# Performance work log

Hardware: AMD Instinct MI355X
Metric: run time of the kernel (lower is better)

## Reference

```python
import jax, jax.numpy as jnp
import numpy as np

N, E, B, T = 50000, 800000, 256, 50
IN_DIM, H, C1, C2, Q_DIM, LH = 128, 4, 32, 128, 32, 128
EPS = 1e-5


def setup_inputs() -> dict:
    key = jax.random.key(0)
    ks = jax.random.split(key, 24)
    g = 0.05
    inp = {
        'x': jax.random.normal(ks[0], (N, IN_DIM), jnp.float32),
        'edge_index': jax.random.randint(ks[1], (2, E), 0, N, jnp.int32),
        'batch': jnp.sort(jax.random.randint(ks[2], (N,), 0, B, jnp.int32)),
        'quant': jax.random.normal(ks[3], (B, T, Q_DIM), jnp.float32),
        # GATConv(128 -> 32, heads=4, concat)
        'gat_W': jax.random.normal(ks[4], (IN_DIM, H * C1), jnp.float32) * g,
        'gat_att_src': jax.random.normal(ks[5], (H, C1), jnp.float32) * g,
        'gat_att_dst': jax.random.normal(ks[6], (H, C1), jnp.float32) * g,
        'gat_b': jnp.zeros((H * C1,), jnp.float32),
        # BN1 over 128 channels (eval mode)
        'bn1_gamma': jnp.ones((H * C1,), jnp.float32),
        'bn1_beta': jnp.zeros((H * C1,), jnp.float32),
        'bn1_mean': jax.random.normal(ks[7], (H * C1,), jnp.float32) * 0.01,
        'bn1_var': jnp.ones((H * C1,), jnp.float32),
        # GCNConv(128 -> 128)
        'gcn_W': jax.random.normal(ks[8], (H * C1, C2), jnp.float32) * g,
        'gcn_b': jnp.zeros((C2,), jnp.float32),
        'bn2_gamma': jnp.ones((C2,), jnp.float32),
        'bn2_beta': jnp.zeros((C2,), jnp.float32),
        'bn2_mean': jax.random.normal(ks[9], (C2,), jnp.float32) * 0.01,
        'bn2_var': jnp.ones((C2,), jnp.float32),
        # GlobalAttention gate: Linear(C2 -> 1)
        'gate_W': jax.random.normal(ks[10], (1, C2), jnp.float32) * g,
        'gate_b': jnp.zeros((1,), jnp.float32),
        # LSTM(Q_DIM -> LH), torch gate order i,f,g,o
        'lstm_Wih': jax.random.normal(ks[11], (4 * LH, Q_DIM), jnp.float32) * g,
        'lstm_Whh': jax.random.normal(ks[12], (4 * LH, LH), jnp.float32) * g,
        'lstm_bih': jnp.zeros((4 * LH,), jnp.float32),
        'lstm_bhh': jnp.zeros((4 * LH,), jnp.float32),
        # final Linear(C2+LH -> 1)
        'fc_W': jax.random.normal(ks[13], (1, C2 + LH), jnp.float32) * g,
        'fc_b': jnp.zeros((1,), jnp.float32),
    }
    return inp


def _segment_softmax(e, seg, num_segments):
    m = jax.ops.segment_max(e, seg, num_segments=num_segments)
    ex = jnp.exp(e - m[seg])
    s = jax.ops.segment_sum(ex, seg, num_segments=num_segments)
    return ex / (s[seg] + 1e-16)


def _bn_eval(x, gamma, beta, mean, var):
    return gamma * (x - mean) * jax.lax.rsqrt(var + EPS) + beta


def _forward(x, edge_index, batch, quant,
             gat_W, gat_att_src, gat_att_dst, gat_b,
             bn1_gamma, bn1_beta, bn1_mean, bn1_var,
             gcn_W, gcn_b, bn2_gamma, bn2_beta, bn2_mean, bn2_var,
             gate_W, gate_b,
             lstm_Wih, lstm_Whh, lstm_bih, lstm_bhh,
             fc_W, fc_b):
    n = x.shape[0]
    loops = jnp.arange(n, dtype=edge_index.dtype)
    ei = jnp.concatenate([edge_index, jnp.stack([loops, loops])], axis=1)  # add self loops
    src, dst = ei[0], ei[1]

    # ---- GATConv ----
    xw = (x @ gat_W).reshape(n, H, C1)                      # [N,H,C1]
    a_src = jnp.sum(xw * gat_att_src, axis=-1)              # [N,H]
    a_dst = jnp.sum(xw * gat_att_dst, axis=-1)
    e = jax.nn.leaky_relu(a_src[src] + a_dst[dst], 0.2)     # [E+N,H]
    alpha = _segment_softmax(e, dst, n)                     # softmax over in-edges per dst
    msg = xw[src] * alpha[:, :, None]                       # [E+N,H,C1]
    h = jax.ops.segment_sum(msg, dst, num_segments=n).reshape(n, H * C1) + gat_b

    h = jax.nn.elu(h)
    h = _bn_eval(h, bn1_gamma, bn1_beta, bn1_mean, bn1_var)

    # ---- GCNConv (sym-normalized with self loops) ----
    deg = jax.ops.segment_sum(jnp.ones_like(dst, jnp.float32), dst, num_segments=n)
    dinv = jnp.where(deg > 0, jax.lax.rsqrt(deg), 0.0)
    norm = dinv[src] * dinv[dst]                            # [E+N]
    hw = h @ gcn_W                                          # [N,C2]
    h2 = jax.ops.segment_sum(hw[src] * norm[:, None], dst, num_segments=n) + gcn_b

    h2 = jax.nn.elu(h2)
    h2 = _bn_eval(h2, bn2_gamma, bn2_beta, bn2_mean, bn2_var)

    # ---- GlobalAttention pooling over graphs ----
    gate = (h2 @ gate_W.T + gate_b)[:, 0]                   # [N]
    score = _segment_softmax(gate, batch, B)
    graph_rep = jax.ops.segment_sum(score[:, None] * h2, batch, num_segments=B)  # [B,C2]

    # ---- LSTM over quant series ----
    def step(carry, xt):
        hh, cc = carry
        gates = xt @ lstm_Wih.T + hh @ lstm_Whh.T + lstm_bih + lstm_bhh
        i, f, gg, o = jnp.split(gates, 4, axis=-1)
        cc = jax.nn.sigmoid(f) * cc + jax.nn.sigmoid(i) * jnp.tanh(gg)
        hh = jax.nn.sigmoid(o) * jnp.tanh(cc)
        return (hh, cc), None

    h0 = jnp.zeros((B, LH), quant.dtype)
    (hT, _), _ = jax.lax.scan(step, (h0, h0), jnp.swapaxes(quant, 0, 1))

    combined = jnp.concatenate([graph_rep, hT], axis=1)     # [B, C2+LH]
    out = (combined @ fc_W.T + fc_b)[:, 0]                  # [B]
    return out


def reference(x, edge_index, batch, quant,
              gat_W, gat_att_src, gat_att_dst, gat_b,
              bn1_gamma, bn1_beta, bn1_mean, bn1_var,
              gcn_W, gcn_b, bn2_gamma, bn2_beta, bn2_mean, bn2_var,
              gate_W, gate_b,
              lstm_Wih, lstm_Whh, lstm_bih, lstm_bhh,
              fc_W, fc_b):
    return _forward(x, edge_index, batch, quant,
                    gat_W, gat_att_src, gat_att_dst, gat_b,
                    bn1_gamma, bn1_beta, bn1_mean, bn1_var,
                    gcn_W, gcn_b, bn2_gamma, bn2_beta, bn2_mean, bn2_var,
                    gate_W, gate_b,
                    lstm_Wih, lstm_Whh, lstm_bih, lstm_bhh,
                    fc_W, fc_b)
```

## Files before the change

### kernel.cpp

```cpp
#include <hip/hip_runtime.h>
#include <cfloat>
#include <cstddef>

constexpr int KIN   = 128;
constexpr int KQD   = 32;
constexpr int KT    = 50;
constexpr int KLH   = 128;
constexpr float BN_EPS = 1e-5f;

typedef __attribute__((ext_vector_type(8))) short bf16x8;
typedef __attribute__((ext_vector_type(4))) float f32x4;
union U8 { bf16x8 v; unsigned u[4]; };

__device__ __forceinline__ float elu_f(float x)  { return x > 0.f ? x : expm1f(x); }
__device__ __forceinline__ float leaky_f(float x){ return x > 0.f ? x : 0.2f * x; }
__device__ __forceinline__ float fsigm(float x)  { return 1.f / (1.f + __expf(-x)); }
__device__ __forceinline__ float ftanh(float x)  { return 1.f - 2.f / (__expf(2.f * x) + 1.f); }

__device__ __forceinline__ unsigned bfpack(float lo, float hi) {
    unsigned ul = __float_as_uint(lo), uh = __float_as_uint(hi);
    ul += 0x7FFFu + ((ul >> 16) & 1u);
    uh += 0x7FFFu + ((uh >> 16) & 1u);
    return (ul >> 16) | (uh & 0xFFFF0000u);
}
__device__ __forceinline__ unsigned short bf1(float v) {
    unsigned u = __float_as_uint(v);
    u += 0x7FFFu + ((u >> 16) & 1u);
    return (unsigned short)(u >> 16);
}
__device__ __forceinline__ float bflo(unsigned u) { return __uint_as_float(u << 16); }
__device__ __forceinline__ float bfhi(unsigned u) { return __uint_as_float(u & 0xFFFF0000u); }

__device__ __forceinline__ bf16x8 pack8(float4 p, float4 q) {
    U8 t;
    t.u[0] = bfpack(p.x, p.y); t.u[1] = bfpack(p.z, p.w);
    t.u[2] = bfpack(q.x, q.y); t.u[3] = bfpack(q.z, q.w);
    return t.v;
}

__global__ void k_deg(const int* __restrict__ ei, int E, int* __restrict__ deg) {
    int e = blockIdx.x * blockDim.x + threadIdx.x;
    if (e < E) atomicAdd(&deg[ei[E + e]], 1);
}

__global__ __launch_bounds__(1024)
void k_scan(const int* __restrict__ deg, int n, int* __restrict__ offsets,
            int* __restrict__ cursor, float* __restrict__ dinv) {
    __shared__ int wsum[16];
    __shared__ int carry_sh;
    int tid = threadIdx.x, lane = tid & 63, w = tid >> 6;
    if (tid == 0) { carry_sh = 0; offsets[0] = 0; }
    __syncthreads();
    for (int base = 0; base < n; base += 4096) {
        int i0 = base + tid * 4;
        int v[4];
        #pragma unroll
        for (int j = 0; j < 4; j++) v[j] = (i0 + j < n) ? deg[i0 + j] : 0;
        int tsum = v[0] + v[1] + v[2] + v[3];
        int sc = tsum;
        #pragma unroll
        for (int d = 1; d < 64; d <<= 1) {
            int o = __shfl_up(sc, d);
            if (lane >= d) sc += o;
        }
        __syncthreads();
        if (lane == 63) wsum[w] = sc;
        __syncthreads();
        if (w == 0) {
            int xx = (lane < 16) ? wsum[lane] : 0;
            #pragma unroll
            for (int d = 1; d < 16; d <<= 1) {
                int o = __shfl_up(xx, d);
                if (lane >= d) xx += o;
            }
            if (lane < 16) wsum[lane] = xx;
        }
        __syncthreads();
        int carry = carry_sh;
        int woff  = (w > 0) ? wsum[w - 1] : 0;
        int run   = carry + woff + sc - tsum;
        #pragma unroll
        for (int j = 0; j < 4; j++) {
            int i = i0 + j;
            if (i < n) {
                cursor[i]      = run;
                offsets[i + 1] = run + v[j];
                dinv[i]        = rsqrtf((float)(v[j] + 1));
                run += v[j];
            }
        }
        __syncthreads();
        if (tid == 0) carry_sh = carry + wsum[15];
    }
}

__global__ void k_fill(const int* __restrict__ ei, int E, int* __restrict__ cursor,
                       int* __restrict__ csr_src) {
    int e = blockIdx.x * blockDim.x + threadIdx.x;
    if (e < E) {
        int s = ei[e], d = ei[E + e];
        int pos = atomicAdd(&cursor[d], 1);
        csr_src[pos] = s;
    }
}

template <bool ATT>
__global__ __launch_bounds__(256, 4)
void k_gemm_mfma(const float* __restrict__ X, const float* __restrict__ W,
                 unsigned* __restrict__ Yb, int nrows,
                 const float* __restrict__ attS, const float* __restrict__ attD,
                 float* __restrict__ a_src, float* __restrict__ a_dst) {
    __shared__ float tile[16][132];
    __shared__ float as_sh[128], ad_sh[128];
    int tid  = threadIdx.x;
    int lane = tid & 63;
    int wv   = tid >> 6;
    if (ATT && tid < 128) { as_sh[tid] = attS[tid]; ad_sh[tid] = attD[tid]; }
    int l16 = lane & 15;
    int kq  = (lane >> 4) * 8;
    bf16x8 bfr[2][4];
    #pragma unroll
    for (int nt = 0; nt < 2; nt++) {
        int n = wv * 32 + nt * 16 + l16;
        #pragma unroll
        for (int kk = 0; kk < 4; kk++) {
            int k0 = kk * 32 + kq;
            float f[8];
            #pragma unroll
            for (int j = 0; j < 8; j++) f[j] = W[(size_t)(k0 + j) * 128 + n];
            U8 t;
            t.u[0] = bfpack(f[0], f[1]); t.u[1] = bfpack(f[2], f[3]);
            t.u[2] = bfpack(f[4], f[5]); t.u[3] = bfpack(f[6], f[7]);
            bfr[nt][kk] = t.v;
        }
    }
    int nch = (nrows + 15) / 16;
    for (int ch = blockIdx.x; ch < nch; ch += gridDim.x) {
        int r0 = ch * 16;
        int r  = r0 + l16;
        bool rok = r < nrows;
        const float* xr = X + (size_t)r * 128 + kq;
        float4 z4 = make_float4(0.f, 0.f, 0.f, 0.f);
        bf16x8 afr[4];
        #pragma unroll
        for (int kk = 0; kk < 4; kk++) {
            float4 p = rok ? *reinterpret_cast<const float4*>(xr + kk * 32)     : z4;
            float4 q = rok ? *reinterpret_cast<const float4*>(xr + kk * 32 + 4) : z4;
            afr[kk] = pack8(p, q);
        }
        f32x4 acc0 = {0.f, 0.f, 0.f, 0.f};
        f32x4 acc1 = {0.f, 0.f, 0.f, 0.f};
        #pragma unroll
        for (int kk = 0; kk < 4; kk++) {
            acc0 = __builtin_amdgcn_mfma_f32_16x16x32_bf16(afr[kk], bfr[0][kk], acc0, 0, 0, 0);
            acc1 = __builtin_amdgcn_mfma_f32_16x16x32_bf16(afr[kk], bfr[1][kk], acc1, 0, 0, 0);
        }
        __syncthreads();
        int rowb = (lane >> 4) * 4;
        int cb   = wv * 32 + l16;
        #pragma unroll
        for (int reg = 0; reg < 4; reg++) {
            tile[rowb + reg][cb]      = acc0[reg];
            tile[rowb + reg][cb + 16] = acc1[reg];
        }
        __syncthreads();
        #pragma unroll
        for (int i = 0; i < 4; i++) {
            int idx = tid + i * 256;
            int row = idx >> 6, cp = idx & 63;
            int rr = r0 + row;
            if (rr < nrows) {
                float2 f = *reinterpret_cast<const float2*>(&tile[row][cp * 2]);
                Yb[(size_t)rr * 64 + cp] = bfpack(f.x, f.y);
            }
        }
        if (ATT && tid < 64) {
            int rr2 = tid >> 2, h = tid & 3;
            if (r0 + rr2 < nrows) {
                float ps = 0.f, pd = 0.f;
                #pragma unroll
                for (int j = 0; j < 32; j++) {
                    float v = tile[rr2][h * 32 + j];
                    ps += v * as_sh[h * 32 + j];
                    pd += v * ad_sh[h * 32 + j];
                }
                a_src[(size_t)(r0 + rr2) * 4 + h] = ps;
                a_dst[(size_t)(r0 + rr2) * 4 + h] = pd;
            }
        }
    }
}

__global__ __launch_bounds__(256)
void k_gat_agg(const int* __restrict__ offsets, const int* __restrict__ csr_src,
               const float* __restrict__ a_src, const float* __restrict__ a_dst,
               const unsigned* __restrict__ xwb, const float* __restrict__ bias,
               const float* __restrict__ g1, const float* __restrict__ b1,
               const float* __restrict__ mu1, const float* __restrict__ var1,
               float* __restrict__ hout, int n) {
    __shared__ int   src_sh[4][64];
    __shared__ float al_sh[4][4][64];
    int lane = threadIdx.x & 63;
    int wv   = threadIdx.x >> 6;
    int wid  = (blockIdx.x * blockDim.x + threadIdx.x) >> 6;
    int nw   = (gridDim.x * blockDim.x) >> 6;
    int hP   = lane >> 4;
    int c0 = lane * 2, c1 = c0 + 1;
    float bi0 = bias[c0], bi1 = bias[c1];
    float A0 = g1[c0] * rsqrtf(var1[c0] + BN_EPS);
    float A1 = g1[c1] * rsqrtf(var1[c1] + BN_EPS);
    float B0 = b1[c0] - mu1[c0] * A0;
    float B1 = b1[c1] - mu1[c1] * A1;
    for (int node = wid; node < n; node += nw) {
        int beg = offsets[node], end = offsets[node + 1];
        int rowlen = end - beg, total = rowlen + 1;
        float4 adv = *reinterpret_cast<const float4*>(&a_dst[(size_t)node * 4]);
        int sv = (lane < rowlen) ? csr_src[beg + lane] : node;
        float4 as4 = *reinterpret_cast<const float4*>(&a_src[(size_t)sv * 4]);
        float e0 = leaky_f(as4.x + adv.x), e1 = leaky_f(as4.y + adv.y);
        float e2 = leaky_f(as4.z + adv.z), e3 = leaky_f(as4.w + adv.w);
        float m[4] = {-FLT_MAX, -FLT_MAX, -FLT_MAX, -FLT_MAX};
        if (lane < total) { m[0] = e0; m[1] = e1; m[2] = e2; m[3] = e3; }
        for (int i = lane + 64; i < total; i += 64) {
            int src = (i < rowlen) ? csr_src[beg + i] : node;
            float4 a4 = *reinterpret_cast<const float4*>(&a_src[(size_t)src * 4]);
            m[0] = fmaxf(m[0], leaky_f(a4.x + adv.x));
            m[1] = fmaxf(m[1], leaky_f(a4.y + adv.y));
            m[2] = fmaxf(m[2], leaky_f(a4.z + adv.z));
            m[3] = fmaxf(m[3], leaky_f(a4.w + adv.w));
        }
        #pragma unroll
        for (int off = 32; off; off >>= 1) {
            #pragma unroll
            for (int h = 0; h < 4; h++) m[h] = fmaxf(m[h], __shfl_xor(m[h], off));
        }
        float ex[4] = {0.f, 0.f, 0.f, 0.f};
        if (lane < total) {
            ex[0] = expf(e0 - m[0]); ex[1] = expf(e1 - m[1]);
            ex[2] = expf(e2 - m[2]); ex[3] = expf(e3 - m[3]);
        }
        float s[4] = {ex[0], ex[1], ex[2], ex[3]};
        for (int i = lane + 64; i < total; i += 64) {
            int src = (i < rowlen) ? csr_src[beg + i] : node;
            float4 a4 = *reinterpret_cast<const float4*>(&a_src[(size_t)src * 4]);
            s[0] += expf(leaky_f(a4.x + adv.x) - m[0]);
            s[1] += expf(leaky_f(a4.y + adv.y) - m[1]);
            s[2] += expf(leaky_f(a4.z + adv.z) - m[2]);
            s[3] += expf(leaky_f(a4.w + adv.w) - m[3]);
        }
        #pragma unroll
        for (int off = 32; off; off >>= 1) {
            #pragma unroll
            for (int h = 0; h < 4; h++) s[h] += __shfl_xor(s[h], off);
        }
        float inv[4];
        #pragma unroll
        for (int h = 0; h < 4; h++) inv[h] = 1.f / (s[h] + 1e-16f);
        src_sh[wv][lane] = sv;
        #pragma unroll
        for (int h = 0; h < 4; h++) al_sh[wv][h][lane] = ex[h] * inv[h];
        __builtin_amdgcn_wave_barrier();
        float acc0 = 0.f, acc1 = 0.f;
        int cnt = min(total, 64);
        {
            int i = 0;
            for (; i + 4 <= cnt; i += 4) {
                int s0 = src_sh[wv][i],     s1 = src_sh[wv][i + 1];
                int s2 = src_sh[wv][i + 2], s3 = src_sh[wv][i + 3];
                float a0 = al_sh[wv][hP][i],     a1 = al_sh[wv][hP][i + 1];
                float a2 = al_sh[wv][hP][i + 2], a3 = al_sh[wv][hP][i + 3];
                unsigned u0 = xwb[(size_t)s0 * 64 + lane];
                unsigned u1 = xwb[(size_t)s1 * 64 + lane];
                unsigned u2 = xwb[(size_t)s2 * 64 + lane];
                unsigned u3 = xwb[(size_t)s3 * 64 + lane];
                acc0 += a0 * bflo(u0); acc1 += a0 * bfhi(u0);
                acc0 += a1 * bflo(u1); acc1 += a1 * bfhi(u1);
                acc0 += a2 * bflo(u2); acc1 += a2 * bfhi(u2);
                acc0 += a3 * bflo(u3); acc1 += a3 * bfhi(u3);
            }
            for (; i < cnt; i++) {
                int src  = src_sh[wv][i];
                float aP = al_sh[wv][hP][i];
                unsigned u = xwb[(size_t)src * 64 + lane];
                acc0 += aP * bflo(u);
                acc1 += aP * bfhi(u);
            }
        }
        for (int base = 64; base < total; base += 64) {
            __builtin_amdgcn_wave_barrier();
            int i = base + lane;
            int src2 = node;
            float a0v = 0.f, a1v = 0.f, a2v = 0.f, a3v = 0.f;
            if (i < total) {
                if (i < rowlen) src2 = csr_src[beg + i];
                float4 a4 = *reinterpret_cast<const float4*>(&a_src[(size_t)src2 * 4]);
                a0v = expf(leaky_f(a4.x + adv.x) - m[0]) * inv[0];
                a1v = expf(leaky_f(a4.y + adv.y) - m[1]) * inv[1];
                a2v = expf(leaky_f(a4.z + adv.z) - m[2]) * inv[2];
                a3v = expf(leaky_f(a4.w + adv.w) - m[3]) * inv[3];
            }
            src_sh[wv][lane] = src2;
            al_sh[wv][0][lane] = a0v; al_sh[wv][1][lane] = a1v;
            al_sh[wv][2][lane] = a2v; al_sh[wv][3][lane] = a3v;
            __builtin_amdgcn_wave_barrier();
            int cnt2 = min(total - base, 64);
            for (int j = 0; j < cnt2; j++) {
                int src  = src_sh[wv][j];
                float aP = al_sh[wv][hP][j];
                unsigned u = xwb[(size_t)src * 64 + lane];
                acc0 += aP * bflo(u);
                acc1 += aP * bfhi(u);
            }
        }
        __builtin_amdgcn_wave_barrier();
        float vA = elu_f(acc0 + bi0);
        float vB = elu_f(acc1 + bi1);
        vA = vA * A0 + B0;
        vB = vB * A1 + B1;
        *reinterpret_cast<float2*>(&hout[(size_t)node * 128 + c0]) =
            make_float2(vA, vB);
    }
}

__global__ __launch_bounds__(256)
void k_gcn_agg(const int* __restrict__ offsets, const int* __restrict__ csr_src,
               const float* __restrict__ dinv, const unsigned* __restrict__ hwb,
               const float* __restrict__ bias,
               const float* __restrict__ g2, const float* __restrict__ b2,
               const float* __restrict__ mu2, const float* __restrict__ var2,
               const float* __restrict__ gateW, const float* __restrict__ gateB,
               float* __restrict__ h2, float* __restrict__ gate, int n) {
    __shared__ int   src_sh[4][64];
    __shared__ float w_sh[4][64];
    int lane = threadIdx.x & 63;
    int wv   = threadIdx.x >> 6;
    int wid  = (blockIdx.x * blockDim.x + threadIdx.x) >> 6;
    int nw   = (gridDim.x * blockDim.x) >> 6;
    int c0 = lane * 2, c1 = c0 + 1;
    float bi0 = bias[c0], bi1 = bias[c1];
    float A0 = g2[c0] * rsqrtf(var2[c0] + BN_EPS);
    float A1 = g2[c1] * rsqrtf(var2[c1] + BN_EPS);
    float B0 = b2[c0] - mu2[c0] * A0;
    float B1 = b2[c1] - mu2[c1] * A1;
    float gw0 = gateW[c0], gw1 = gateW[c1], gB = gateB[0];
    for (int node = wid; node < n; node += nw) {
        int beg = offsets[node], end = offsets[node + 1];
        int rowlen = end - beg;
        float dn = dinv[node];
        unsigned us = hwb[(size_t)node * 64 + lane];
        float acc0 = dn * dn * bflo(us);
        float acc1 = dn * dn * bfhi(us);
        for (int base = 0; base < rowlen; base += 64) {
            __builtin_amdgcn_wave_barrier();
            int i = base + lane;
            int src2 = node;
            float wv2 = 0.f;
            if (i < rowlen) { src2 = csr_src[beg + i]; wv2 = dinv[src2] * dn; }
            src_sh[wv][lane] = src2;
            w_sh[wv][lane]   = wv2;
            __builtin_amdgcn_wave_barrier();
            int cnt = min(rowlen - base, 64);
            int j = 0;
            for (; j + 4 <= cnt; j += 4) {
                int s0 = src_sh[wv][j],     s1 = src_sh[wv][j + 1];
                int s2 = src_sh[wv][j + 2], s3 = src_sh[wv][j + 3];
                float w0 = w_sh[wv][j],     w1 = w_sh[wv][j + 1];
                float w2 = w_sh[wv][j + 2], w3 = w_sh[wv][j + 3];
                unsigned u0 = hwb[(size_t)s0 * 64 + lane];
                unsigned u1 = hwb[(size_t)s1 * 64 + lane];
                unsigned u2 = hwb[(size_t)s2 * 64 + lane];
                unsigned u3 = hwb[(size_t)s3 * 64 + lane];
                acc0 += w0 * bflo(u0); acc1 += w0 * bfhi(u0);
                acc0 += w1 * bflo(u1); acc1 += w1 * bfhi(u1);
                acc0 += w2 * bflo(u2); acc1 += w2 * bfhi(u2);
                acc0 += w3 * bflo(u3); acc1 += w3 * bfhi(u3);
            }
            for (; j < cnt; j++) {
                int src = src_sh[wv][j];
                float w = w_sh[wv][j];
                unsigned u = hwb[(size_t)src * 64 + lane];
                acc0 += w * bflo(u);
                acc1 += w * bfhi(u);
            }
        }
        __builtin_amdgcn_wave_barrier();
        float vA = elu_f(acc0 + bi0);
        float vB = elu_f(acc1 + bi1);
        vA = vA * A0 + B0;
        vB = vB * A1 + B1;
        *reinterpret_cast<float2*>(&h2[(size_t)node * 128 + c0]) =
            make_float2(vA, vB);
        float p = vA * gw0 + vB * gw1;
        #pragma unroll
        for (int off = 32; off; off >>= 1) p += __shfl_xor(p, off);
        if (lane == 0) gate[node] = p + gB;
    }
}

__device__ __forceinline__ int lbound(const int* a, int n, int key) {
    int lo = 0, hi = n;
    while (lo < hi) { int mid = (lo + hi) >> 1; if (a[mid] < key) lo = mid + 1; else hi = mid; }
    return lo;
}

__global__ __launch_bounds__(256)
void k_pool(const int* __restrict__ batch, const float* __restrict__ gate,
            const float* __restrict__ h2, const float* __restrict__ hT,
            const float* __restrict__ fcW, const float* __restrict__ fcB,
            float* __restrict__ out, int n) {
    int b = blockIdx.x, tid = threadIdx.x;
    __shared__ float red[256];
    __shared__ float sc_sh[256];
    int start = lbound(batch, n, b);
    int end   = lbound(batch, n, b + 1);
    float m = -FLT_MAX;
    for (int i = start + tid; i < end; i += 256) m = fmaxf(m, gate[i]);
    red[tid] = m; __syncthreads();
    for (int s2 = 128; s2 > 0; s2 >>= 1) {
        if (tid < s2) red[tid] = fmaxf(red[tid], red[tid + s2]);
        __syncthreads();
    }
    m = red[0]; __syncthreads();
    float s = 0.f;
    for (int i = start + tid; i < end; i += 256) s += expf(gate[i] - m);
    red[tid] = s; __syncthreads();
    for (int s2 = 128; s2 > 0; s2 >>= 1) {
        if (tid < s2) red[tid] += red[tid + s2];
        __syncthreads();
    }
    float inv = 1.f / (red[0] + 1e-16f);
    __syncthreads();
    int j = tid & 127, half = tid >> 7;
    float acc = 0.f;
    for (int base = start; base < end; base += 256) {
        int cnt = min(256, end - base);
        __syncthreads();
        if (tid < cnt) sc_sh[tid] = expf(gate[base + tid] - m) * inv;
        __syncthreads();
        for (int ii = half; ii < cnt; ii += 2)
            acc += sc_sh[ii] * h2[(size_t)(base + ii) * 128 + j];
    }
    red[tid] = acc; __syncthreads();
    if (half == 0) sc_sh[j] = red[j] + red[128 + j];
    __syncthreads();
    float p = 0.f;
    if (tid < 128)
        p = fcW[tid] * sc_sh[tid] + fcW[128 + tid] * hT[(size_t)b * 128 + tid];
    red[tid] = p; __syncthreads();
    for (int s2 = 128; s2 > 0; s2 >>= 1) {
        if (tid < s2) red[tid] += red[tid + s2];
        __syncthreads();
    }
    if (tid == 0) out[b] = red[0] + fcB[0];
}

__global__ __launch_bounds__(512)
void k_lstm_mfma(const float* __restrict__ quant, const float* __restrict__ Wih,
                 const float* __restrict__ Whh, const float* __restrict__ bih,
                 const float* __restrict__ bhh, float* __restrict__ hstate) {
    __shared__ unsigned short h16[2][16][136];
    __shared__ unsigned short x16[16][1608];
    int t = threadIdx.x, lane = t & 63, w = t >> 6;
    int b0   = blockIdx.x * 16;
    int l15  = lane & 15;
    int kq8  = (lane >> 4) * 8;
    int j    = w * 16 + l15;
    int rowq = (lane >> 4) * 4;
    float bi_i = bih[j]       + bhh[j];
    float bi_f = bih[128 + j] + bhh[128 + j];
    float bi_g = bih[256 + j] + bhh[256 + j];
    float bi_o = bih[384 + j] + bhh[384 + j];
    bf16x8 whh_f[4][4], wih_f[4];
    #pragma unroll
    for (int c = 0; c < 4; c++) {
        int col = c * 128 + j;
        #pragma unroll
        for (int kk = 0; kk < 4; kk++) {
            const float* wr = &Whh[(size_t)col * 128 + kk * 32 + kq8];
            whh_f[c][kk] = pack8(*reinterpret_cast<const float4*>(wr),
                                 *reinterpret_cast<const float4*>(wr + 4));
        }
        const float* wr = &Wih[(size_t)col * 32 + kq8];
        wih_f[c] = pack8(*reinterpret_cast<const float4*>(wr),
                         *reinterpret_cast<const float4*>(wr + 4));
    }
    unsigned* xw32 = reinterpret_cast<unsigned*>(&x16[0][0]);
    for (int p = t; p < 16 * 800; p += 512) {
        int r = p / 800, rem = p - r * 800;
        float2 f = *reinterpret_cast<const float2*>(
            &quant[(size_t)(b0 + r) * (KT * KQD) + rem * 2]);
        xw32[r * 804 + rem] = bfpack(f.x, f.y);
    }
    for (int p = t; p < 16 * 136; p += 512) {
        int r = p / 136, cc = p - r * 136;
        h16[0][r][cc] = 0;
    }
    float cst[4] = {0.f, 0.f, 0.f, 0.f};
    int cur = 0;
    __syncthreads();
    for (int s = 0; s < KT; s++) {
        bf16x8 ah[4];
        #pragma unroll
        for (int kk = 0; kk < 4; kk++)
            ah[kk] = *reinterpret_cast<const bf16x8*>(&h16[cur][l15][kk * 32 + kq8]);
        bf16x8 ax = *reinterpret_cast<const bf16x8*>(&x16[l15][s * 32 + kq8]);
        f32x4 ai = {0.f,0.f,0.f,0.f}, af = {0.f,0.f,0.f,0.f};
        f32x4 ag = {0.f,0.f,0.f,0.f}, ao = {0.f,0.f,0.f,0.f};
        #pragma unroll
        for (int kk = 0; kk < 4; kk++) {
            ai = __builtin_amdgcn_mfma_f32_16x16x32_bf16(ah[kk], whh_f[0][kk], ai, 0, 0, 0);
            af = __builtin_amdgcn_mfma_f32_16x16x32_bf16(ah[kk], whh_f[1][kk], af, 0, 0, 0);
            ag = __builtin_amdgcn_mfma_f32_16x16x32_bf16(ah[kk], whh_f[2][kk], ag, 0, 0, 0);
            ao = __builtin_amdgcn_mfma_f32_16x16x32_bf16(ah[kk], whh_f[3][kk], ao, 0, 0, 0);
        }
        ai = __builtin_amdgcn_mfma_f32_16x16x32_bf16(ax, wih_f[0], ai, 0, 0, 0);
        af = __builtin_amdgcn_mfma_f32_16x16x32_bf16(ax, wih_f[1], af, 0, 0, 0);
        ag = __builtin_amdgcn_mfma_f32_16x16x32_bf16(ax, wih_f[2], ag, 0, 0, 0);
        ao = __builtin_amdgcn_mfma_f32_16x16x32_bf16(ax, wih_f[3], ao, 0, 0, 0);
        int nxt = cur ^ 1;
        #pragma unroll
        for (int r = 0; r < 4; r++) {
            float ig = fsigm(ai[r] + bi_i);
            float fg = fsigm(af[r] + bi_f);
            float gg = ftanh(ag[r] + bi_g);
            float og = fsigm(ao[r] + bi_o);
            cst[r] = fg * cst[r] + ig * gg;
            h16[nxt][rowq + r][j] = bf1(og * ftanh(cst[r]));
        }
        __syncthreads();
        cur = nxt;
    }
    for (int p = t; p < 16 * KLH; p += 512) {
        int row = p >> 7, jj = p & 127;
        hstate[(size_t)(b0 + row) * KLH + jj] =
            __uint_as_float((unsigned)h16[cur][row][jj] << 16);
    }
}

extern "C" void kernel_launch(void* const* d_in, const int* in_sizes, int n_in,
                              void* d_out, int out_size, void* d_ws, size_t ws_size,
                              hipStream_t stream) {
    const float* x     = (const float*)d_in[0];
    const int*   ei    = (const int*)  d_in[1];
    const int*   batch = (const int*)  d_in[2];
    const float* quant = (const float*)d_in[3];
    const float* gatW  = (const float*)d_in[4];
    const float* attS  = (const float*)d_in[5];
    const float* attD  = (const float*)d_in[6];
    const float* gatB  = (const float*)d_in[7];
    const float* bn1g  = (const float*)d_in[8];
    const float* bn1b  = (const float*)d_in[9];
    const float* bn1m  = (const float*)d_in[10];
    const float* bn1v  = (const float*)d_in[11];
    const float* gcnW  = (const float*)d_in[12];
    const float* gcnB  = (const float*)d_in[13];
    const float* bn2g  = (const float*)d_in[14];
    const float* bn2b  = (const float*)d_in[15];
    const float* bn2m  = (const float*)d_in[16];
    const float* bn2v  = (const float*)d_in[17];
    const float* gateW = (const float*)d_in[18];
    const float* gateB = (const float*)d_in[19];
    const float* Wih   = (const float*)d_in[20];
    const float* Whh   = (const float*)d_in[21];
    const float* bih   = (const float*)d_in[22];
    const float* bhh   = (const float*)d_in[23];
    const float* fcW   = (const float*)d_in[24];
    const float* fcB   = (const float*)d_in[25];

    int N = in_sizes[0] / KIN;
    int E = in_sizes[1] / 2;
    int B = in_sizes[3] / (KT * KQD);

    char* ws = (char*)d_ws;
    size_t off = 0;
    auto alloc = [&](size_t bytes) -> void* {
        void* p = ws + off;
        off += (bytes + 511) & ~(size_t)511;
        return p;
    };
    int*      deg     = (int*)     alloc((size_t)N * 4);
    int*      offsets = (int*)     alloc((size_t)(N + 1) * 4);
    int*      cursor  = (int*)     alloc((size_t)N * 4);
    float*    dinv    = (float*)   alloc((size_t)N * 4);
    int*      csr_src = (int*)     alloc((size_t)E * 4);
    float*    a_src   = (float*)   alloc((size_t)N * 16);
    float*    a_dst   = (float*)   alloc((size_t)N * 16);
    unsigned* xwb     = (unsigned*)alloc((size_t)N * 256);
    float*    hbuf    = (float*)   alloc((size_t)N * 512);
    float*    gate    = (float*)   alloc((size_t)N * 4);
    float*    hstate  = (float*)   alloc((size_t)B * KLH * 4);

    hipMemsetAsync(deg, 0, (size_t)N * 4, stream);
    int eb = (E + 255) / 256;
    k_deg <<<eb, 256, 0, stream>>>(ei, E, deg);
    k_scan<<<1, 1024, 0, stream>>>(deg, N, offsets, cursor, dinv);
    k_fill<<<eb, 256, 0, stream>>>(ei, E, cursor, csr_src);

    k_lstm_mfma<<<B / 16, 512, 0, stream>>>(quant, Wih, Whh, bih, bhh, hstate);

    k_gemm_mfma<true ><<<512, 256, 0, stream>>>(x, gatW, xwb, N, attS, attD, a_src, a_dst);
    k_gat_agg<<<2048, 256, 0, stream>>>(offsets, csr_src, a_src, a_dst, xwb, gatB,
                                        bn1g, bn1b, bn1m, bn1v, hbuf, N);
    k_gemm_mfma<false><<<512, 256, 0, stream>>>(hbuf, gcnW, xwb, N,
                                                nullptr, nullptr, nullptr, nullptr);
    k_gcn_agg<<<2048, 256, 0, stream>>>(offsets, csr_src, dinv, xwb, gcnB,
                                        bn2g, bn2b, bn2m, bn2v, gateW, gateB,
                                        hbuf, gate, N);
    k_pool<<<B, 256, 0, stream>>>(batch, gate, hbuf, hstate, fcW, fcB,
                                  (float*)d_out, N);
}
```

Before: 467.1 us.

## Parallelize CSR prefix scan, shorten LSTM MFMA chain, enlarge aggregation grids

The single-block serial degree scan becomes a three-kernel multi-block scan: per-block sums, a tiny serial scan over the block sums, then a per-block local scan. In the LSTM loop, the input projection for step s+1 is computed ahead of time, and each gate's recurrent MFMA chain is split into two independent accumulators so the dependent chain per step is shorter. The GAT and GCN aggregation grids grow from 2048 to 3072 blocks. The cost is two extra kernel launches, and a small change in floating-point summation order in the LSTM gates.

```diff
diff --git a/kernel.cpp b/kernel.cpp
--- a/kernel.cpp
+++ b/kernel.cpp
@@ -44,54 +44,73 @@
 }
 
 __global__ __launch_bounds__(1024)
-void k_scan(const int* __restrict__ deg, int n, int* __restrict__ offsets,
-            int* __restrict__ cursor, float* __restrict__ dinv) {
+void k_scan_a(const int* __restrict__ deg, int n, int* __restrict__ bsum) {
     __shared__ int wsum[16];
-    __shared__ int carry_sh;
     int tid = threadIdx.x, lane = tid & 63, w = tid >> 6;
-    if (tid == 0) { carry_sh = 0; offsets[0] = 0; }
+    int i0 = blockIdx.x * 4096 + tid * 4;
+    int t = 0;
+    #pragma unroll
+    for (int j = 0; j < 4; j++) t += (i0 + j < n) ? deg[i0 + j] : 0;
+    #pragma unroll
+    for (int d = 1; d < 64; d <<= 1) t += __shfl_xor(t, d);
+    if (lane == 0) wsum[w] = t;
     __syncthreads();
-    for (int base = 0; base < n; base += 4096) {
-        int i0 = base + tid * 4;
-        int v[4];
-        #pragma unroll
-        for (int j = 0; j < 4; j++) v[j] = (i0 + j < n) ? deg[i0 + j] : 0;
-        int tsum = v[0] + v[1] + v[2] + v[3];
-        int sc = tsum;
-        #pragma unroll
-        for (int d = 1; d < 64; d <<= 1) {
-            int o = __shfl_up(sc, d);
-            if (lane >= d) sc += o;
-        }
-        __syncthreads();
-        if (lane == 63) wsum[w] = sc;
-        __syncthreads();
-        if (w == 0) {
-            int xx = (lane < 16) ? wsum[lane] : 0;
-            #pragma unroll
-            for (int d = 1; d < 16; d <<= 1) {
-                int o = __shfl_up(xx, d);
-                if (lane >= d) xx += o;
-            }
-            if (lane < 16) wsum[lane] = xx;
-        }
-        __syncthreads();
-        int carry = carry_sh;
-        int woff  = (w > 0) ? wsum[w - 1] : 0;
-        int run   = carry + woff + sc - tsum;
-        #pragma unroll
-        for (int j = 0; j < 4; j++) {
-            int i = i0 + j;
-            if (i < n) {
-                cursor[i]      = run;
-                offsets[i + 1] = run + v[j];
-                dinv[i]        = rsqrtf((float)(v[j] + 1));
-                run += v[j];
-            }
-        }
-        __syncthreads();
-        if (tid == 0) carry_sh = carry + wsum[15];
-    }
+    if (tid == 0) {
+        int s = 0;
+        #pragma unroll
+        for (int k = 0; k < 16; k++) s += wsum[k];
+        bsum[blockIdx.x] = s;
+    }
+}
+
+__global__ void k_scan_b(int* __restrict__ bsum, int nb) {
+    if (threadIdx.x == 0) {
+        int run = 0;
+        for (int i = 0; i < nb; i++) { int v = bsum[i]; bsum[i] = run; run += v; }
+    }
+}
+
+__global__ __launch_bounds__(1024)
+void k_scan_c(const int* __restrict__ deg, int n, const int* __restrict__ bsum,
+              int* __restrict__ offsets, int* __restrict__ cursor,
+              float* __restrict__ dinv) {
+    __shared__ int wsum[16];
+    int tid = threadIdx.x, lane = tid & 63, w = tid >> 6;
+    int i0 = blockIdx.x * 4096 + tid * 4;
+    int v[4];
+    #pragma unroll
+    for (int j = 0; j < 4; j++) v[j] = (i0 + j < n) ? deg[i0 + j] : 0;
+    int tsum = v[0] + v[1] + v[2] + v[3];
+    int sc = tsum;
+    #pragma unroll
+    for (int d = 1; d < 64; d <<= 1) {
+        int o = __shfl_up(sc, d);
+        if (lane >= d) sc += o;
+    }
+    if (lane == 63) wsum[w] = sc;
+    __syncthreads();
+    if (w == 0) {
+        int xx = (lane < 16) ? wsum[lane] : 0;
+        #pragma unroll
+        for (int d = 1; d < 16; d <<= 1) {
+            int o = __shfl_up(xx, d);
+            if (lane >= d) xx += o;
+        }
+        if (lane < 16) wsum[lane] = xx;
+    }
+    __syncthreads();
+    int run = bsum[blockIdx.x] + ((w > 0) ? wsum[w - 1] : 0) + sc - tsum;
+    #pragma unroll
+    for (int j = 0; j < 4; j++) {
+        int i = i0 + j;
+        if (i < n) {
+            cursor[i]      = run;
+            offsets[i + 1] = run + v[j];
+            dinv[i]        = rsqrtf((float)(v[j] + 1));
+            run += v[j];
+        }
+    }
+    if (blockIdx.x == 0 && tid == 0) offsets[0] = 0;
 }
 
 __global__ void k_fill(const int* __restrict__ ei, int E, int* __restrict__ cursor,
@@ -498,34 +517,47 @@
     float cst[4] = {0.f, 0.f, 0.f, 0.f};
     int cur = 0;
     __syncthreads();
+    f32x4 xg[4];
+    {
+        bf16x8 ax = *reinterpret_cast<const bf16x8*>(&x16[l15][kq8]);
+        #pragma unroll
+        for (int c = 0; c < 4; c++) {
+            f32x4 z = {0.f, 0.f, 0.f, 0.f};
+            xg[c] = __builtin_amdgcn_mfma_f32_16x16x32_bf16(ax, wih_f[c], z, 0, 0, 0);
+        }
+    }
     for (int s = 0; s < KT; s++) {
-        bf16x8 ah[4];
-        #pragma unroll
-        for (int kk = 0; kk < 4; kk++)
-            ah[kk] = *reinterpret_cast<const bf16x8*>(&h16[cur][l15][kk * 32 + kq8]);
-        bf16x8 ax = *reinterpret_cast<const bf16x8*>(&x16[l15][s * 32 + kq8]);
-        f32x4 ai = {0.f,0.f,0.f,0.f}, af = {0.f,0.f,0.f,0.f};
-        f32x4 ag = {0.f,0.f,0.f,0.f}, ao = {0.f,0.f,0.f,0.f};
-        #pragma unroll
-        for (int kk = 0; kk < 4; kk++) {
-            ai = __builtin_amdgcn_mfma_f32_16x16x32_bf16(ah[kk], whh_f[0][kk], ai, 0, 0, 0);
-            af = __builtin_amdgcn_mfma_f32_16x16x32_bf16(ah[kk], whh_f[1][kk], af, 0, 0, 0);
-            ag = __builtin_amdgcn_mfma_f32_16x16x32_bf16(ah[kk], whh_f[2][kk], ag, 0, 0, 0);
-            ao = __builtin_amdgcn_mfma_f32_16x16x32_bf16(ah[kk], whh_f[3][kk], ao, 0, 0, 0);
-        }
-        ai = __builtin_amdgcn_mfma_f32_16x16x32_bf16(ax, wih_f[0], ai, 0, 0, 0);
-        af = __builtin_amdgcn_mfma_f32_16x16x32_bf16(ax, wih_f[1], af, 0, 0, 0);
-        ag = __builtin_amdgcn_mfma_f32_16x16x32_bf16(ax, wih_f[2], ag, 0, 0, 0);
-        ao = __builtin_amdgcn_mfma_f32_16x16x32_bf16(ax, wih_f[3], ao, 0, 0, 0);
+        bf16x8 ah0 = *reinterpret_cast<const bf16x8*>(&h16[cur][l15][kq8]);
+        bf16x8 ah1 = *reinterpret_cast<const bf16x8*>(&h16[cur][l15][32 + kq8]);
+        bf16x8 ah2 = *reinterpret_cast<const bf16x8*>(&h16[cur][l15][64 + kq8]);
+        bf16x8 ah3 = *reinterpret_cast<const bf16x8*>(&h16[cur][l15][96 + kq8]);
+        f32x4 ga[4], gb[4];
+        #pragma unroll
+        for (int c = 0; c < 4; c++) {
+            f32x4 z = {0.f, 0.f, 0.f, 0.f};
+            f32x4 a = __builtin_amdgcn_mfma_f32_16x16x32_bf16(ah0, whh_f[c][0], xg[c], 0, 0, 0);
+            a = __builtin_amdgcn_mfma_f32_16x16x32_bf16(ah1, whh_f[c][1], a, 0, 0, 0);
+            f32x4 b = __builtin_amdgcn_mfma_f32_16x16x32_bf16(ah2, whh_f[c][2], z, 0, 0, 0);
+            b = __builtin_amdgcn_mfma_f32_16x16x32_bf16(ah3, whh_f[c][3], b, 0, 0, 0);
+            ga[c] = a; gb[c] = b;
+        }
         int nxt = cur ^ 1;
         #pragma unroll
         for (int r = 0; r < 4; r++) {
-            float ig = fsigm(ai[r] + bi_i);
-            float fg = fsigm(af[r] + bi_f);
-            float gg = ftanh(ag[r] + bi_g);
-            float og = fsigm(ao[r] + bi_o);
+            float ig = fsigm(ga[0][r] + gb[0][r] + bi_i);
+            float fg = fsigm(ga[1][r] + gb[1][r] + bi_f);
+            float gg = ftanh(ga[2][r] + gb[2][r] + bi_g);
+            float og = fsigm(ga[3][r] + gb[3][r] + bi_o);
             cst[r] = fg * cst[r] + ig * gg;
             h16[nxt][rowq + r][j] = bf1(og * ftanh(cst[r]));
+        }
+        if (s + 1 < KT) {
+            bf16x8 ax = *reinterpret_cast<const bf16x8*>(&x16[l15][(s + 1) * 32 + kq8]);
+            #pragma unroll
+            for (int c = 0; c < 4; c++) {
+                f32x4 z = {0.f, 0.f, 0.f, 0.f};
+                xg[c] = __builtin_amdgcn_mfma_f32_16x16x32_bf16(ax, wih_f[c], z, 0, 0, 0);
+            }
         }
         __syncthreads();
         cur = nxt;
@@ -578,11 +610,13 @@
         off += (bytes + 511) & ~(size_t)511;
         return p;
     };
+    int nb = (N + 4095) / 4096;
     int*      deg     = (int*)     alloc((size_t)N * 4);
     int*      offsets = (int*)     alloc((size_t)(N + 1) * 4);
     int*      cursor  = (int*)     alloc((size_t)N * 4);
     float*    dinv    = (float*)   alloc((size_t)N * 4);
     int*      csr_src = (int*)     alloc((size_t)E * 4);
+    int*      bsum    = (int*)     alloc((size_t)nb * 4);
     float*    a_src   = (float*)   alloc((size_t)N * 16);
     float*    a_dst   = (float*)   alloc((size_t)N * 16);
     unsigned* xwb     = (unsigned*)alloc((size_t)N * 256);
@@ -592,18 +626,20 @@
 
     hipMemsetAsync(deg, 0, (size_t)N * 4, stream);
     int eb = (E + 255) / 256;
-    k_deg <<<eb, 256, 0, stream>>>(ei, E, deg);
-    k_scan<<<1, 1024, 0, stream>>>(deg, N, offsets, cursor, dinv);
-    k_fill<<<eb, 256, 0, stream>>>(ei, E, cursor, csr_src);
+    k_deg   <<<eb, 256, 0, stream>>>(ei, E, deg);
+    k_scan_a<<<nb, 1024, 0, stream>>>(deg, N, bsum);
+    k_scan_b<<<1, 64, 0, stream>>>(bsum, nb);
+    k_scan_c<<<nb, 1024, 0, stream>>>(deg, N, bsum, offsets, cursor, dinv);
+    k_fill  <<<eb, 256, 0, stream>>>(ei, E, cursor, csr_src);
 
     k_lstm_mfma<<<B / 16, 512, 0, stream>>>(quant, Wih, Whh, bih, bhh, hstate);
 
     k_gemm_mfma<true ><<<512, 256, 0, stream>>>(x, gatW, xwb, N, attS, attD, a_src, a_dst);
-    k_gat_agg<<<2048, 256, 0, stream>>>(offsets, csr_src, a_src, a_dst, xwb, gatB,
+    k_gat_agg<<<3072, 256, 0, stream>>>(offsets, csr_src, a_src, a_dst, xwb, gatB,
                                         bn1g, bn1b, bn1m, bn1v, hbuf, N);
     k_gemm_mfma<false><<<512, 256, 0, stream>>>(hbuf, gcnW, xwb, N,
                                                 nullptr, nullptr, nullptr, nullptr);
-    k_gcn_agg<<<2048, 256, 0, stream>>>(offsets, csr_src, dinv, xwb, gcnB,
+    k_gcn_agg<<<3072, 256, 0, stream>>>(offsets, csr_src, dinv, xwb, gcnB,
                                         bn2g, bn2b, bn2m, bn2v, gateW, gateB,
                                         hbuf, gate, N);
     k_pool<<<B, 256, 0, stream>>>(batch, gate, hbuf, hstate, fcW, fcB,
```

After: 430.3 us. 7.9% less time.
